# Optimization experiments

Measured on AMD Instinct MI355X. Metric: run time of the kernel, lower is better.

## Reference

```python
import jax, jax.numpy as jnp
import numpy as np

INPUT_SIZE = 1024
HIDDEN_SIZE = 1024


def setup_inputs() -> dict:
    key = jax.random.key(0)
    k1, k2, k3, k4, k5 = jax.random.split(key, 5)
    B, S, D, H = 64, 512, INPUT_SIZE, HIDDEN_SIZE
    bound_x = 1.0 / np.sqrt(D)
    bound_h = 1.0 / np.sqrt(H)
    # nn.Linear weights: (out, in) layout, uniform(-1/sqrt(in), 1/sqrt(in))
    Wx = jax.random.uniform(k1, (4 * H, D), jnp.float32, -bound_x, bound_x)
    bx = jax.random.uniform(k2, (4 * H,), jnp.float32, -bound_x, bound_x)
    Wh = jax.random.uniform(k3, (4 * H, H), jnp.float32, -bound_h, bound_h)
    bh = jax.random.uniform(k4, (4 * H,), jnp.float32, -bound_h, bound_h)
    x = jax.random.normal(k5, (B, S, D), jnp.float32)
    return {"x": x, "Wx": Wx, "bx": bx, "Wh": Wh, "bh": bh}


def _lstm_forward(x, Wx, bx, Wh, bh):
    B, S, D = x.shape
    H = Wh.shape[1]
    # Precompute the input projection for all timesteps in one big GEMM.
    x_gates = jnp.einsum('bsd,gd->bsg', x, Wx) + bx + bh  # (B, S, 4H)

    def step(carry, xg_t):
        h, c = carry
        gates = xg_t + h @ Wh.T  # (B, 4H)
        i, f, o, g = jnp.split(gates, 4, axis=1)
        i = jax.nn.sigmoid(i)
        f = jax.nn.sigmoid(f)
        o = jax.nn.sigmoid(o)
        g = jnp.tanh(g)
        c_new = f * c + i * g
        h_new = o * jnp.tanh(c_new)
        return (h_new, c_new), h_new

    h0 = jnp.zeros((B, H), x.dtype)
    c0 = jnp.zeros((B, H), x.dtype)
    (h_last, c_last), hs = jax.lax.scan(step, (h0, c0), jnp.swapaxes(x_gates, 0, 1))
    outputs = jnp.swapaxes(hs, 0, 1)  # (B, S, H)
    return outputs, (h_last, c_last)


def reference(x, Wx, bx, Wh, bh):
    return _lstm_forward(x, Wx, bx, Wh, bh)
```

## Files before the change

kernel.cpp:

```cpp
#include <hip/hip_runtime.h>


typedef short short8 __attribute__((ext_vector_type(8)));
typedef float float4v __attribute__((ext_vector_type(4)));
typedef unsigned long long u64;

__device__ __forceinline__ short f2bf(float f) {
  union { float f; unsigned u; } v; v.f = f;
  unsigned r = (v.u + 0x7fffu + ((v.u >> 16) & 1u)) >> 16;
  return (short)r;
}

__device__ __forceinline__ float sigm(float z) {
  float e = __expf(-fabsf(z));
  float p = 1.0f / (1.0f + e);
  return z >= 0.0f ? p : 1.0f - p;
}

__device__ __forceinline__ float tanh_s(float z) {
  float e = __expf(-2.0f * fabsf(z));
  float r = (1.0f - e) / (1.0f + e);
  return z >= 0.0f ? r : -r;
}

__global__ __launch_bounds__(256) void xconv(const float* __restrict__ x,
                                             short* __restrict__ xbf) {
  const int gid = blockIdx.x * 256 + threadIdx.x;
  const long i8 = (long)gid * 8;
  const int d  = (int)(i8 & 1023);
  const int bs = (int)(i8 >> 10);
  const int s  = bs & 511;
  const int b  = bs >> 9;
  const float4v* src = (const float4v*)(x + i8);
  float4v v0 = src[0], v1 = src[1];
  short8 o;
  o[0]=f2bf(v0[0]); o[1]=f2bf(v0[1]); o[2]=f2bf(v0[2]); o[3]=f2bf(v0[3]);
  o[4]=f2bf(v1[0]); o[5]=f2bf(v1[1]); o[6]=f2bf(v1[2]); o[7]=f2bf(v1[3]);
  *(short8*)(xbf + (((size_t)(s * 64 + b)) << 10) + d) = o;
}

template <bool XBF>
__global__ __launch_bounds__(1024, 4) void lstm_persist(
    const float* __restrict__ x, const short* __restrict__ xbf,
    const float* __restrict__ Wx, const float* __restrict__ bx,
    const float* __restrict__ Wh, const float* __restrict__ bh,
    float* __restrict__ out, unsigned* cnt, short* hbuf)
{
  __shared__ short hS[32 * 1024];
  __shared__ float red[4][32][68];
  __shared__ unsigned flag;

  const int tid  = threadIdx.x;
  const int bid  = blockIdx.x;
  const int g    = bid & 1;
  const int js   = bid >> 1;
  const int lane = tid & 63;
  const int w    = tid >> 6;
  const int kq   = w >> 2;
  const int rg   = w & 3;
  const int l15  = lane & 15;
  const int lh   = lane >> 4;

  unsigned* cnt_g = cnt + g * 64;
  short* hb_g = hbuf + (size_t)g * 65536;

  short8 bw[16];
  {
    const int gi  = l15 & 3;
    const int jj  = l15 >> 2;
    const int row = gi * 1024 + js * 16 + rg * 4 + jj;
    const float* Wsrc = (kq < 2) ? (Wx + (size_t)row * 1024 + kq * 512)
                                 : (Wh + (size_t)row * 1024 + (kq - 2) * 512);
    #pragma unroll
    for (int ks = 0; ks < 16; ++ks) {
      const float* p = Wsrc + ks * 32 + lh * 8;
      float4v v0 = *(const float4v*)p;
      float4v v1 = *(const float4v*)(p + 4);
      short8 o;
      o[0]=f2bf(v0[0]); o[1]=f2bf(v0[1]); o[2]=f2bf(v0[2]); o[3]=f2bf(v0[3]);
      o[4]=f2bf(v1[0]); o[5]=f2bf(v1[1]); o[6]=f2bf(v1[2]); o[7]=f2bf(v1[3]);
      bw[ks] = o;
    }
  }

  const int eb  = tid >> 4;
  const int ejj = tid & 15;
  const int jg  = js * 16 + ejj;
  float bias[4] = {0.f, 0.f, 0.f, 0.f};
  if (tid < 512) {
    #pragma unroll
    for (int gi = 0; gi < 4; ++gi) bias[gi] = bx[gi * 1024 + jg] + bh[gi * 1024 + jg];
  }
  float c_reg = 0.0f, h_keep = 0.0f;

  if (tid == 0)
    __hip_atomic_store(&flag, 0u, __ATOMIC_RELAXED, __HIP_MEMORY_SCOPE_WORKGROUP);
  __syncthreads();

  char* const hSB = (char*)hS;

  for (int t = 0; t < 512; ++t) {
    float4v acc[2];
    acc[0] = (float4v){0.f, 0.f, 0.f, 0.f};
    acc[1] = (float4v){0.f, 0.f, 0.f, 0.f};

    if (kq < 2) {
      if (XBF) {
        const short* xb = xbf + ((size_t)t << 16) + kq * 512 + lh * 8;
        #pragma unroll
        for (int ks = 0; ks < 16; ++ks) {
          #pragma unroll
          for (int mt = 0; mt < 2; ++mt) {
            const int b = g * 32 + mt * 16 + l15;
            short8 a = *(const short8*)(xb + ((size_t)b << 10) + ks * 32);
            acc[mt] = __builtin_amdgcn_mfma_f32_16x16x32_bf16(a, bw[ks], acc[mt], 0, 0, 0);
          }
        }
      } else {
        const float* Ab = x + (size_t)t * 1024 + kq * 512 + lh * 8;
        #pragma unroll
        for (int ks = 0; ks < 16; ++ks) {
          #pragma unroll
          for (int mt = 0; mt < 2; ++mt) {
            const int b = g * 32 + mt * 16 + l15;
            const float* p = Ab + (size_t)b * 524288 + ks * 32;
            float4v v0 = *(const float4v*)p;
            float4v v1 = *(const float4v*)(p + 4);
            short8 a;
            a[0]=f2bf(v0[0]); a[1]=f2bf(v0[1]); a[2]=f2bf(v0[2]); a[3]=f2bf(v0[3]);
            a[4]=f2bf(v1[0]); a[5]=f2bf(v1[1]); a[6]=f2bf(v1[2]); a[7]=f2bf(v1[3]);
            acc[mt] = __builtin_amdgcn_mfma_f32_16x16x32_bf16(a, bw[ks], acc[mt], 0, 0, 0);
          }
        }
      }
      #pragma unroll
      for (int mt = 0; mt < 2; ++mt)
        #pragma unroll
        for (int r = 0; r < 4; ++r)
          red[kq][mt * 16 + lh * 4 + r][rg * 16 + l15] = acc[mt][r];
    } else {
      if (w == 8) {
        const unsigned target = (unsigned)t * 64u;
        while (__hip_atomic_load(cnt_g, __ATOMIC_RELAXED, __HIP_MEMORY_SCOPE_AGENT) < target)
          __builtin_amdgcn_s_sleep(2);
        if (lane == 0)
          __hip_atomic_store(&flag, (unsigned)(t + 1), __ATOMIC_RELAXED, __HIP_MEMORY_SCOPE_WORKGROUP);
      } else {
        while (__hip_atomic_load(&flag, __ATOMIC_RELAXED, __HIP_MEMORY_SCOPE_WORKGROUP) < (unsigned)(t + 1))
          __builtin_amdgcn_s_sleep(1);
      }
      const int tau = tid - 512;
      const int row = tau >> 4;
      const int sec = tau & 15;
      const short* src = hb_g + (size_t)(t & 1) * 32768 + row * 1024 + sec * 8;
      #pragma unroll
      for (int i = 0; i < 8; ++i) {
        const u64* p = (const u64*)(src + i * 128);
        union { u64 q[2]; short8 s; } u;
        u.q[0] = __hip_atomic_load(p,     __ATOMIC_RELAXED, __HIP_MEMORY_SCOPE_AGENT);
        u.q[1] = __hip_atomic_load(p + 1, __ATOMIC_RELAXED, __HIP_MEMORY_SCOPE_AGENT);
        const unsigned byte = (((unsigned)row << 11) + sec * 16 + i * 256)
                              ^ ((unsigned)(row & 7) << 4);
        *(short8*)(hSB + byte) = u.s;
      }
    }
    __syncthreads();

    if (kq >= 2) {
      const unsigned cb = (unsigned)((kq - 2) * 1024 + lh * 16);
      const unsigned xr = (unsigned)((l15 & 7) << 4);
      #pragma unroll
      for (int ks = 0; ks < 16; ++ks) {
        #pragma unroll
        for (int mt = 0; mt < 2; ++mt) {
          const unsigned byte = (((unsigned)(mt * 16 + l15) << 11) + cb + ks * 64) ^ xr;
          short8 a = *(const short8*)(hSB + byte);
          acc[mt] = __builtin_amdgcn_mfma_f32_16x16x32_bf16(a, bw[ks], acc[mt], 0, 0, 0);
        }
      }
      #pragma unroll
      for (int mt = 0; mt < 2; ++mt)
        #pragma unroll
        for (int r = 0; r < 4; ++r)
          red[kq][mt * 16 + lh * 4 + r][rg * 16 + l15] = acc[mt][r];
    }
    __syncthreads();

    if (tid < 512) {
      const int base = (ejj >> 2) * 16 + (ejj & 3) * 4;
      const float4v r0 = *(const float4v*)&red[0][eb][base];
      const float4v r1 = *(const float4v*)&red[1][eb][base];
      const float4v r2 = *(const float4v*)&red[2][eb][base];
      const float4v r3 = *(const float4v*)&red[3][eb][base];
      const float s0 = r0[0] + r1[0] + r2[0] + r3[0] + bias[0];
      const float s1 = r0[1] + r1[1] + r2[1] + r3[1] + bias[1];
      const float s2 = r0[2] + r1[2] + r2[2] + r3[2] + bias[2];
      const float s3 = r0[3] + r1[3] + r2[3] + r3[3] + bias[3];
      const float ig = sigm(s0);
      const float fg = sigm(s1);
      const float og = sigm(s2);
      const float gg = tanh_s(s3);
      c_reg = fg * c_reg + ig * gg;
      const float hh = og * tanh_s(c_reg);
      h_keep = hh;
      out[((size_t)(g * 32 + eb) * 512 + t) * 1024 + jg] = hh;
      unsigned hv = (unsigned)(unsigned short)f2bf(hh);
      unsigned nb = (unsigned)__shfl_xor((int)hv, 1, 64);
      if ((ejj & 1) == 0) {
        unsigned vv = hv | (nb << 16);
        unsigned* dst = (unsigned*)(hb_g + (size_t)((t + 1) & 1) * 32768 + eb * 1024 + jg);
        __hip_atomic_store(dst, vv, __ATOMIC_RELAXED, __HIP_MEMORY_SCOPE_AGENT);
      }
    }
    __syncthreads();
    if (tid == 0)
      __hip_atomic_fetch_add(cnt_g, 1u, __ATOMIC_RELAXED, __HIP_MEMORY_SCOPE_AGENT);
  }

  if (tid < 512) {
    const size_t BSH = (size_t)64 * 512 * 1024;
    out[BSH + (size_t)(g * 32 + eb) * 1024 + jg] = h_keep;
    out[BSH + 65536 + (size_t)(g * 32 + eb) * 1024 + jg] = c_reg;
  }
}

extern "C" void kernel_launch(void* const* d_in, const int* in_sizes, int n_in,
                              void* d_out, int out_size, void* d_ws, size_t ws_size,
                              hipStream_t stream) {
  (void)in_sizes; (void)n_in; (void)out_size;
  const float* x  = (const float*)d_in[0];
  const float* Wx = (const float*)d_in[1];
  const float* bx = (const float*)d_in[2];
  const float* Wh = (const float*)d_in[3];
  const float* bh = (const float*)d_in[4];
  float* out = (float*)d_out;

  unsigned* cnt = (unsigned*)d_ws;
  short* hbuf   = (short*)((char*)d_ws + 1024);
  short* xbf    = (short*)((char*)d_ws + 1024 + 262144);
  const size_t need_xbf = 1024u + 262144u + (size_t)64 * 512 * 1024 * 2;

  hipMemsetAsync(d_ws, 0, 1024 + 262144, stream);

  if (ws_size >= need_xbf) {
    hipLaunchKernelGGL(xconv, dim3(16384), dim3(256), 0, stream, x, xbf);
    hipLaunchKernelGGL(lstm_persist<true>, dim3(128), dim3(1024), 0, stream,
                       x, xbf, Wx, bx, Wh, bh, out, cnt, hbuf);
  } else {
    hipLaunchKernelGGL(lstm_persist<false>, dim3(128), dim3(1024), 0, stream,
                       x, hbuf, Wx, bx, Wh, bh, out, cnt, hbuf);
  }
}
```

Measured before the change: 7.471 ms.

## Replace global step counter with per-wave readiness slots and incremental h gathering

Each producer wave now publishes its own per-step flag slot instead of one block-level atomic counter. Consumer waves poll those slots with a ballot and copy each 16-column chunk of h into shared memory as soon as its producers are ready, rather than waiting for all 64 blocks. The output store moves after the flag publish so it stays off the critical path. This aims to cut the recurrence sync latency of the persistent LSTM, but adds more polling traffic and relies on ordering via an explicit vmcnt wait with relaxed atomics.

```diff
diff --git a/kernel.cpp b/kernel.cpp
--- a/kernel.cpp
+++ b/kernel.cpp
@@ -44,11 +44,10 @@
     const float* __restrict__ x, const short* __restrict__ xbf,
     const float* __restrict__ Wx, const float* __restrict__ bx,
     const float* __restrict__ Wh, const float* __restrict__ bh,
-    float* __restrict__ out, unsigned* cnt, short* hbuf)
+    float* __restrict__ out, unsigned* slots, short* hbuf)
 {
   __shared__ short hS[32 * 1024];
   __shared__ float red[4][32][68];
-  __shared__ unsigned flag;
 
   const int tid  = threadIdx.x;
   const int bid  = blockIdx.x;
@@ -61,7 +60,7 @@
   const int l15  = lane & 15;
   const int lh   = lane >> 4;
 
-  unsigned* cnt_g = cnt + g * 64;
+  unsigned* slot_g = slots + g * 512;
   short* hb_g = hbuf + (size_t)g * 65536;
 
   short8 bw[16];
@@ -93,9 +92,9 @@
   }
   float c_reg = 0.0f, h_keep = 0.0f;
 
-  if (tid == 0)
-    __hip_atomic_store(&flag, 0u, __ATOMIC_RELAXED, __HIP_MEMORY_SCOPE_WORKGROUP);
-  __syncthreads();
+  const int pbase = (w - 8) * 8;
+  const int srow  = lane >> 1;
+  const int shalf = lane & 1;
 
   char* const hSB = (char*)hS;
 
@@ -139,29 +138,28 @@
         for (int r = 0; r < 4; ++r)
           red[kq][mt * 16 + lh * 4 + r][rg * 16 + l15] = acc[mt][r];
     } else {
-      if (w == 8) {
-        const unsigned target = (unsigned)t * 64u;
-        while (__hip_atomic_load(cnt_g, __ATOMIC_RELAXED, __HIP_MEMORY_SCOPE_AGENT) < target)
-          __builtin_amdgcn_s_sleep(2);
-        if (lane == 0)
-          __hip_atomic_store(&flag, (unsigned)(t + 1), __ATOMIC_RELAXED, __HIP_MEMORY_SCOPE_WORKGROUP);
-      } else {
-        while (__hip_atomic_load(&flag, __ATOMIC_RELAXED, __HIP_MEMORY_SCOPE_WORKGROUP) < (unsigned)(t + 1))
-          __builtin_amdgcn_s_sleep(1);
-      }
-      const int tau = tid - 512;
-      const int row = tau >> 4;
-      const int sec = tau & 15;
-      const short* src = hb_g + (size_t)(t & 1) * 32768 + row * 1024 + sec * 8;
-      #pragma unroll
-      for (int i = 0; i < 8; ++i) {
-        const u64* p = (const u64*)(src + i * 128);
-        union { u64 q[2]; short8 s; } u;
-        u.q[0] = __hip_atomic_load(p,     __ATOMIC_RELAXED, __HIP_MEMORY_SCOPE_AGENT);
-        u.q[1] = __hip_atomic_load(p + 1, __ATOMIC_RELAXED, __HIP_MEMORY_SCOPE_AGENT);
-        const unsigned byte = (((unsigned)row << 11) + sec * 16 + i * 256)
-                              ^ ((unsigned)(row & 7) << 4);
-        *(short8*)(hSB + byte) = u.s;
+      const unsigned target = (unsigned)t;
+      const short* hb = hb_g + (size_t)(t & 1) * 32768;
+      const unsigned* sp = slot_g + (pbase << 3) + lane;
+      unsigned got = 0;
+      while (got != 0xFFu) {
+        const unsigned v = __hip_atomic_load(sp, __ATOMIC_RELAXED, __HIP_MEMORY_SCOPE_AGENT);
+        const unsigned long long rdy = __ballot(v >= target);
+        #pragma unroll
+        for (int p = 0; p < 8; ++p) {
+          if (!(got & (1u << p)) && (((rdy >> (p * 8)) & 0xFFull) == 0xFFull)) {
+            const int jp = pbase + p;
+            const u64* q = (const u64*)(hb + srow * 1024 + jp * 16 + shalf * 8);
+            union { u64 u[2]; short8 s; } uu;
+            uu.u[0] = __hip_atomic_load(q,     __ATOMIC_RELAXED, __HIP_MEMORY_SCOPE_AGENT);
+            uu.u[1] = __hip_atomic_load(q + 1, __ATOMIC_RELAXED, __HIP_MEMORY_SCOPE_AGENT);
+            unsigned byte = ((unsigned)srow << 11) + (unsigned)(jp * 32 + shalf * 16);
+            byte ^= ((unsigned)(srow & 7) << 4);
+            *(short8*)(hSB + byte) = uu.s;
+            got |= 1u << p;
+          }
+        }
+        if (got != 0xFFu) __builtin_amdgcn_s_sleep(1);
       }
     }
     __syncthreads();
@@ -203,7 +201,6 @@
       c_reg = fg * c_reg + ig * gg;
       const float hh = og * tanh_s(c_reg);
       h_keep = hh;
-      out[((size_t)(g * 32 + eb) * 512 + t) * 1024 + jg] = hh;
       unsigned hv = (unsigned)(unsigned short)f2bf(hh);
       unsigned nb = (unsigned)__shfl_xor((int)hv, 1, 64);
       if ((ejj & 1) == 0) {
@@ -211,10 +208,13 @@
         unsigned* dst = (unsigned*)(hb_g + (size_t)((t + 1) & 1) * 32768 + eb * 1024 + jg);
         __hip_atomic_store(dst, vv, __ATOMIC_RELAXED, __HIP_MEMORY_SCOPE_AGENT);
       }
+      asm volatile("s_waitcnt vmcnt(0)" ::: "memory");
+      if (lane == 0)
+        __hip_atomic_store(slot_g + js * 8 + w, (unsigned)(t + 1),
+                           __ATOMIC_RELAXED, __HIP_MEMORY_SCOPE_AGENT);
+      out[((size_t)(g * 32 + eb) * 512 + t) * 1024 + jg] = hh;
     }
     __syncthreads();
-    if (tid == 0)
-      __hip_atomic_fetch_add(cnt_g, 1u, __ATOMIC_RELAXED, __HIP_MEMORY_SCOPE_AGENT);
   }
 
   if (tid < 512) {
@@ -235,19 +235,19 @@
   const float* bh = (const float*)d_in[4];
   float* out = (float*)d_out;
 
-  unsigned* cnt = (unsigned*)d_ws;
-  short* hbuf   = (short*)((char*)d_ws + 1024);
-  short* xbf    = (short*)((char*)d_ws + 1024 + 262144);
-  const size_t need_xbf = 1024u + 262144u + (size_t)64 * 512 * 1024 * 2;
-
-  hipMemsetAsync(d_ws, 0, 1024 + 262144, stream);
+  unsigned* slots = (unsigned*)d_ws;
+  short* hbuf     = (short*)((char*)d_ws + 8192);
+  short* xbf      = (short*)((char*)d_ws + 8192 + 262144);
+  const size_t need_xbf = 8192u + 262144u + (size_t)64 * 512 * 1024 * 2;
+
+  hipMemsetAsync(d_ws, 0, 8192 + 262144, stream);
 
   if (ws_size >= need_xbf) {
     hipLaunchKernelGGL(xconv, dim3(16384), dim3(256), 0, stream, x, xbf);
     hipLaunchKernelGGL(lstm_persist<true>, dim3(128), dim3(1024), 0, stream,
-                       x, xbf, Wx, bx, Wh, bh, out, cnt, hbuf);
+                       x, xbf, Wx, bx, Wh, bh, out, slots, hbuf);
   } else {
     hipLaunchKernelGGL(lstm_persist<false>, dim3(128), dim3(1024), 0, stream,
-                       x, hbuf, Wx, bx, Wh, bh, out, cnt, hbuf);
-  }
-}
+                       x, hbuf, Wx, bx, Wh, bh, out, slots, hbuf);
+  }
+}
```

Measured after the change: 9.195 ms. +23.1%, slower.

## Replace atomic counter barrier with per-block flag slots and ballot polling

Applied to the files above, without the earlier changes.

The single shared atomic counter per group is replaced with per-block slot words. Every waiting wave polls all 64 slots with one lane each and a ballot, instead of one wave polling the counter and relaying a shared-memory flag. Each gate wave counts its own arrival in shared memory once its h stores have drained, and wave 15 then publishes the block's step in its slot, so the end-of-step __syncthreads is gone. The output store now happens after the h publish so it stays off the critical path. The cost is more polling traffic across 64 slots and more subtle memory-ordering assumptions.

```diff
diff --git a/kernel.cpp b/kernel.cpp
--- a/kernel.cpp
+++ b/kernel.cpp
@@ -44,11 +44,11 @@
     const float* __restrict__ x, const short* __restrict__ xbf,
     const float* __restrict__ Wx, const float* __restrict__ bx,
     const float* __restrict__ Wh, const float* __restrict__ bh,
-    float* __restrict__ out, unsigned* cnt, short* hbuf)
+    float* __restrict__ out, unsigned* slots, short* hbuf)
 {
   __shared__ short hS[32 * 1024];
   __shared__ float red[4][32][68];
-  __shared__ unsigned flag;
+  __shared__ unsigned arrive;
 
   const int tid  = threadIdx.x;
   const int bid  = blockIdx.x;
@@ -61,7 +61,7 @@
   const int l15  = lane & 15;
   const int lh   = lane >> 4;
 
-  unsigned* cnt_g = cnt + g * 64;
+  unsigned* slot_g = slots + g * 1024;
   short* hb_g = hbuf + (size_t)g * 65536;
 
   short8 bw[16];
@@ -94,7 +94,7 @@
   float c_reg = 0.0f, h_keep = 0.0f;
 
   if (tid == 0)
-    __hip_atomic_store(&flag, 0u, __ATOMIC_RELAXED, __HIP_MEMORY_SCOPE_WORKGROUP);
+    __hip_atomic_store(&arrive, 0u, __ATOMIC_RELAXED, __HIP_MEMORY_SCOPE_WORKGROUP);
   __syncthreads();
 
   char* const hSB = (char*)hS;
@@ -139,15 +139,14 @@
         for (int r = 0; r < 4; ++r)
           red[kq][mt * 16 + lh * 4 + r][rg * 16 + l15] = acc[mt][r];
     } else {
-      if (w == 8) {
-        const unsigned target = (unsigned)t * 64u;
-        while (__hip_atomic_load(cnt_g, __ATOMIC_RELAXED, __HIP_MEMORY_SCOPE_AGENT) < target)
-          __builtin_amdgcn_s_sleep(2);
-        if (lane == 0)
-          __hip_atomic_store(&flag, (unsigned)(t + 1), __ATOMIC_RELAXED, __HIP_MEMORY_SCOPE_WORKGROUP);
-      } else {
-        while (__hip_atomic_load(&flag, __ATOMIC_RELAXED, __HIP_MEMORY_SCOPE_WORKGROUP) < (unsigned)(t + 1))
+      const unsigned target = (unsigned)t;
+      {
+        const unsigned* sp = slot_g + (size_t)lane * 16;
+        for (;;) {
+          const unsigned v = __hip_atomic_load(sp, __ATOMIC_RELAXED, __HIP_MEMORY_SCOPE_AGENT);
+          if (__ballot(v >= target) == ~0ull) break;
           __builtin_amdgcn_s_sleep(1);
+        }
       }
       const int tau = tid - 512;
       const int row = tau >> 4;
@@ -203,7 +202,6 @@
       c_reg = fg * c_reg + ig * gg;
       const float hh = og * tanh_s(c_reg);
       h_keep = hh;
-      out[((size_t)(g * 32 + eb) * 512 + t) * 1024 + jg] = hh;
       unsigned hv = (unsigned)(unsigned short)f2bf(hh);
       unsigned nb = (unsigned)__shfl_xor((int)hv, 1, 64);
       if ((ejj & 1) == 0) {
@@ -211,10 +209,18 @@
         unsigned* dst = (unsigned*)(hb_g + (size_t)((t + 1) & 1) * 32768 + eb * 1024 + jg);
         __hip_atomic_store(dst, vv, __ATOMIC_RELAXED, __HIP_MEMORY_SCOPE_AGENT);
       }
-    }
-    __syncthreads();
-    if (tid == 0)
-      __hip_atomic_fetch_add(cnt_g, 1u, __ATOMIC_RELAXED, __HIP_MEMORY_SCOPE_AGENT);
+      asm volatile("s_waitcnt vmcnt(0)" ::: "memory");
+      if (lane == 0)
+        __hip_atomic_fetch_add(&arrive, 1u, __ATOMIC_RELAXED, __HIP_MEMORY_SCOPE_WORKGROUP);
+      out[((size_t)(g * 32 + eb) * 512 + t) * 1024 + jg] = hh;
+    } else if (w == 15) {
+      const unsigned tgt = 8u * (unsigned)(t + 1);
+      while (__hip_atomic_load(&arrive, __ATOMIC_RELAXED, __HIP_MEMORY_SCOPE_WORKGROUP) < tgt)
+        __builtin_amdgcn_s_sleep(1);
+      if (lane == 0)
+        __hip_atomic_store(slot_g + (size_t)js * 16, (unsigned)(t + 1),
+                           __ATOMIC_RELAXED, __HIP_MEMORY_SCOPE_AGENT);
+    }
   }
 
   if (tid < 512) {
@@ -235,19 +241,19 @@
   const float* bh = (const float*)d_in[4];
   float* out = (float*)d_out;
 
-  unsigned* cnt = (unsigned*)d_ws;
-  short* hbuf   = (short*)((char*)d_ws + 1024);
-  short* xbf    = (short*)((char*)d_ws + 1024 + 262144);
-  const size_t need_xbf = 1024u + 262144u + (size_t)64 * 512 * 1024 * 2;
-
-  hipMemsetAsync(d_ws, 0, 1024 + 262144, stream);
+  unsigned* slots = (unsigned*)d_ws;
+  short* hbuf     = (short*)((char*)d_ws + 8192);
+  short* xbf      = (short*)((char*)d_ws + 8192 + 262144);
+  const size_t need_xbf = 8192u + 262144u + (size_t)64 * 512 * 1024 * 2;
+
+  hipMemsetAsync(d_ws, 0, 8192 + 262144, stream);
 
   if (ws_size >= need_xbf) {
     hipLaunchKernelGGL(xconv, dim3(16384), dim3(256), 0, stream, x, xbf);
     hipLaunchKernelGGL(lstm_persist<true>, dim3(128), dim3(1024), 0, stream,
-                       x, xbf, Wx, bx, Wh, bh, out, cnt, hbuf);
+                       x, xbf, Wx, bx, Wh, bh, out, slots, hbuf);
   } else {
     hipLaunchKernelGGL(lstm_persist<false>, dim3(128), dim3(1024), 0, stream,
-                       x, hbuf, Wx, bx, Wh, bh, out, cnt, hbuf);
-  }
-}
+                       x, hbuf, Wx, bx, Wh, bh, out, slots, hbuf);
+  }
+}
```

Result: slower. 7.822 ms (+4.7%).
